# Kernel optimization log

Measured on AMD Instinct MI355X. Metric: run time of the kernel, lower is better.

## Reference

```python
import jax, jax.numpy as jnp
import numpy as np

EPS = 1e-5  # torch BatchNorm2d default eps
K = 3       # kernel_size
D = 1       # dilation (== padding)


def setup_inputs() -> dict:
    key = jax.random.key(0)
    k0, k1, k2 = jax.random.split(key, 3)
    N, C, H, W, O = 4, 2048, 32, 32, 256
    return {
        "x": jax.random.normal(k0, (N, C, H, W), jnp.float32),
        "conv_w": jax.random.normal(k1, (K * K, C, K, K), jnp.float32) * 0.01,
        "gamma": jnp.ones((K * K,), jnp.float32),
        "beta": jnp.zeros((K * K,), jnp.float32),
        "weight": jax.random.normal(k2, (O, C, K * K), jnp.float32) * 0.01,
    }


def reference(x, conv_w, gamma, beta, weight):
    n, c, h, w = x.shape
    # --- dynamic-kernel generator: conv (stride 1, pad=dilation) -> BN (train mode) -> softmax over K*K ---
    sigma = jax.lax.conv_general_dilated(
        x, conv_w, window_strides=(1, 1), padding=[(D, D), (D, D)],
        rhs_dilation=(D, D), dimension_numbers=("NCHW", "OIHW", "NCHW"))  # (n, K*K, h, w)
    mean = sigma.mean(axis=(0, 2, 3), keepdims=True)
    var = sigma.var(axis=(0, 2, 3), keepdims=True)  # biased variance, as torch BN uses for normalization
    sigma = (sigma - mean) * jax.lax.rsqrt(var + EPS)
    sigma = sigma * gamma[None, :, None, None] + beta[None, :, None, None]
    sigma = jax.nn.softmax(sigma, axis=1)            # softmax over the K*K kernel positions
    sigma = sigma.reshape(n, K * K, h * w)           # (n, K*K, h*w)
    # --- unfold (im2col), channel-major (C, kh, kw) ordering matching torch F.unfold ---
    patches = jax.lax.conv_general_dilated_patches(
        x, (K, K), (1, 1), [(D, D), (D, D)], rhs_dilation=(D, D),
        dimension_numbers=("NCHW", "OIHW", "NCHW"))  # (n, C*K*K, h, w)
    patches = patches.reshape(n, c, K * K, h * w)     # (n, C, K*K, h*w)
    # --- per-pixel dynamic weighting + learned projection ---
    # out[n,o,m] = sum_{c,l} patches[n,c,l,m] * sigma[n,l,m] * weight[o,c,l]
    out = jnp.einsum("nclm,nlm,ocl->nom", patches, sigma, weight)
    return out.reshape(n, weight.shape[0], h, w)
```

## Files before the change

### kernel.cpp

```cpp
#include <hip/hip_runtime.h>
#include <hip/hip_bf16.h>
#include <stdint.h>

typedef unsigned short u16;
typedef __attribute__((ext_vector_type(8))) short short8;
typedef __attribute__((ext_vector_type(4))) float floatx4;

#define N_IMG 4
#define C_IN  2048
#define HW    1024
#define KK    9
#define O_OUT 256
#define NPIX  4096
#define M_ROWS 2385
#define M_PAD  2432
#define K_DIM  2048
#define BN_EPS 1e-5f

#define OFF_A    0u
#define OFF_XT   9961472u
#define OFF_H    26738688u
#define OFF_SRAW 46661632u
#define OFF_SIG  46809088u
#define OFF_STAT 46956544u

__device__ __forceinline__ u16 f2b(float f) {
    unsigned u = __float_as_uint(f);
    return (u16)((u + 0x7FFFu + ((u >> 16) & 1u)) >> 16);
}

__device__ __forceinline__ void load8f(const float* base, size_t eidx, u16* out) {
    const float* p = base + eidx;
    float4 a = ((const float4*)p)[0];
    float4 b = ((const float4*)p)[1];
    float f[8] = {a.x, a.y, a.z, a.w, b.x, b.y, b.z, b.w};
#pragma unroll
    for (int j = 0; j < 8; ++j) out[j] = f2b(f[j]);
}

__global__ void build_xt(const float* __restrict__ x, u16* __restrict__ xt) {
    __shared__ __align__(16) u16 lds[64 * 72];
    int c0 = blockIdx.x * 64, p0 = blockIdx.y * 64, n = blockIdx.z;
    int t = threadIdx.x;
    int r = t >> 3, pv = (t & 7) * 8;
    u16 h0[8], h1[8];
    load8f(x, (size_t)(n * C_IN + c0 + r) * HW + p0 + pv, h0);
    load8f(x, (size_t)(n * C_IN + c0 + r + 32) * HW + p0 + pv, h1);
#pragma unroll
    for (int j = 0; j < 8; ++j) {
        lds[(pv + j) * 72 + r]      = h0[j];
        lds[(pv + j) * 72 + r + 32] = h1[j];
    }
    __syncthreads();
    int pr = t >> 3, cv = (t & 7) * 8;
    uint4 o0 = *(const uint4*)&lds[pr * 72 + cv];
    uint4 o1 = *(const uint4*)&lds[(pr + 32) * 72 + cv];
    *(uint4*)(xt + (size_t)(n * HW + p0 + pr) * K_DIM + c0 + cv) = o0;
    *(uint4*)(xt + (size_t)(n * HW + p0 + pr + 32) * K_DIM + c0 + cv) = o1;
}

__global__ void build_a(const float* __restrict__ wgt, const float* __restrict__ cw,
                        u16* __restrict__ A, float* __restrict__ stats) {
    __shared__ __align__(16) u16 lds[9 * 2056];
    int b = blockIdx.x, t = threadIdx.x;
    if (b < 256) {
        size_t base = (size_t)b * 18432;
        for (int i = 0; i < 9; ++i) {
            int e0 = (t + i * 256) * 8;
            u16 hv[8];
            load8f(wgt, base + e0, hv);
#pragma unroll
            for (int j = 0; j < 8; ++j) {
                int e = e0 + j;
                int c = e / 9, l = e - c * 9;
                lds[l * 2056 + c] = hv[j];
            }
        }
        __syncthreads();
        for (int l = 0; l < 9; ++l) {
            size_t row = (size_t)l * 256 + b;
            *(uint4*)(A + row * K_DIM + t * 8) = *(const uint4*)&lds[l * 2056 + t * 8];
        }
    } else if (b < 265) {
        int l = b - 256;
        size_t base = (size_t)l * 18432;
        for (int i = 0; i < 9; ++i) {
            int e0 = (t + i * 256) * 8;
            u16 hv[8];
            load8f(cw, base + e0, hv);
#pragma unroll
            for (int j = 0; j < 8; ++j) {
                int e = e0 + j;
                int c = e / 9, k = e - c * 9;
                lds[k * 2056 + c] = hv[j];
            }
        }
        __syncthreads();
        for (int k = 0; k < 9; ++k) {
            size_t row = 2304 + (size_t)k * 9 + l;
            *(uint4*)(A + row * K_DIM + t * 8) = *(const uint4*)&lds[k * 2056 + t * 8];
        }
    } else {
        uint4 z = {0, 0, 0, 0};
        uint4* dst = (uint4*)(A + (size_t)2385 * K_DIM);
        for (int i = t; i < (47 * 2048) / 8; i += 256) dst[i] = z;
        if (t < 18) stats[t] = 0.0f;
    }
}

__device__ __forceinline__ void gload_lds16(const void* g, void* l) {
    __builtin_amdgcn_global_load_lds((__attribute__((address_space(1))) void*)(g),
                                     (__attribute__((address_space(3))) void*)(l), 16, 0, 0);
}

__global__ void gemm_bt(const u16* __restrict__ A, const u16* __restrict__ B,
                        __hip_bfloat16* __restrict__ C) {
    __shared__ __align__(16) u16 As[128 * 32];
    __shared__ __align__(16) u16 Bs[128 * 32];
    int bx = blockIdx.x;
    int mt = bx % 19, nt = bx / 19;
    int m0 = mt * 128, n0 = nt * 128;
    int t = threadIdx.x;
    int w = t >> 6, lam = t & 63;
    int wm = w >> 1, wn = w & 1;
    int lm = lam & 15, q = lam >> 4;

    floatx4 acc[4][4];
    floatx4 z = {0.f, 0.f, 0.f, 0.f};
#pragma unroll
    for (int i = 0; i < 4; ++i)
#pragma unroll
        for (int j = 0; j < 4; ++j) acc[i][j] = z;

    int c0 = w, c1 = w + 4;
    int rrow0 = c0 * 16 + (lam >> 2);
    int rrow1 = c1 * 16 + (lam >> 2);
    int kc = (lam & 3) * 8;
    const u16* gA0 = A + (size_t)(m0 + rrow0) * K_DIM + kc;
    const u16* gA1 = A + (size_t)(m0 + rrow1) * K_DIM + kc;
    const u16* gB0 = B + (size_t)(n0 + rrow0) * K_DIM + kc;
    const u16* gB1 = B + (size_t)(n0 + rrow1) * K_DIM + kc;
    u16* lA0 = As + c0 * 512;  u16* lA1 = As + c1 * 512;
    u16* lB0 = Bs + c0 * 512;  u16* lB1 = Bs + c1 * 512;

    for (int kt = 0; kt < K_DIM / 32; ++kt) {
        gload_lds16(gA0, lA0);
        gload_lds16(gA1, lA1);
        gload_lds16(gB0, lB0);
        gload_lds16(gB1, lB1);
        gA0 += 32; gA1 += 32; gB0 += 32; gB1 += 32;
        __syncthreads();
        short8 af[4], bf[4];
#pragma unroll
        for (int i = 0; i < 4; ++i)
            af[i] = *(const short8*)(As + (wm * 64 + i * 16 + lm) * 32 + q * 8);
#pragma unroll
        for (int j = 0; j < 4; ++j)
            bf[j] = *(const short8*)(Bs + (wn * 64 + j * 16 + lm) * 32 + q * 8);
#pragma unroll
        for (int i = 0; i < 4; ++i)
#pragma unroll
            for (int j = 0; j < 4; ++j)
                acc[i][j] = __builtin_amdgcn_mfma_f32_16x16x32_bf16(af[i], bf[j], acc[i][j], 0, 0, 0);
        __syncthreads();
    }
#pragma unroll
    for (int i = 0; i < 4; ++i) {
        int gm = m0 + wm * 64 + i * 16 + q * 4;
#pragma unroll
        for (int j = 0; j < 4; ++j) {
            int gn = n0 + wn * 64 + j * 16 + lm;
#pragma unroll
            for (int r = 0; r < 4; ++r)
                C[(size_t)(gm + r) * NPIX + gn] = __float2bfloat16(acc[i][j][r]);
        }
    }
}

__global__ void sigma_stats(const __hip_bfloat16* __restrict__ Hm, float* __restrict__ sraw,
                            float* __restrict__ stats) {
    int b = blockIdx.x;
    int n = b / 9, l = b - n * 9;
    int t = threadIdx.x;
    float s1 = 0.f, s2 = 0.f;
    for (int i = 0; i < 4; ++i) {
        int pix = t + i * 256;
        int y = pix >> 5, x = pix & 31;
        float v = 0.f;
#pragma unroll
        for (int k = 0; k < 9; ++k) {
            int yy = y + k / 3 - 1, xx = x + (k % 3) - 1;
            if (yy >= 0 && yy < 32 && xx >= 0 && xx < 32)
                v += __bfloat162float(Hm[(size_t)(2304 + k * 9 + l) * NPIX + n * HW + yy * 32 + xx]);
        }
        sraw[(size_t)b * HW + pix] = v;
        s1 += v; s2 += v * v;
    }
    __shared__ float r1[256], r2[256];
    r1[t] = s1; r2[t] = s2;
    __syncthreads();
    for (int s = 128; s > 0; s >>= 1) {
        if (t < s) { r1[t] += r1[t + s]; r2[t] += r2[t + s]; }
        __syncthreads();
    }
    if (t == 0) { atomicAdd(&stats[l], r1[0]); atomicAdd(&stats[9 + l], r2[0]); }
}

__global__ void bn_softmax(const float* __restrict__ sraw, const float* __restrict__ stats,
                           const float* __restrict__ gamma, const float* __restrict__ beta,
                           float* __restrict__ sig) {
    int gid = blockIdx.x * 256 + threadIdx.x;
    int n = gid >> 10, pix = gid & 1023;
    float v[9];
    float mx = -1e30f;
#pragma unroll
    for (int l = 0; l < 9; ++l) {
        float mean = stats[l] * (1.f / 4096.f);
        float var  = stats[9 + l] * (1.f / 4096.f) - mean * mean;
        float tv = (sraw[(size_t)(n * 9 + l) * HW + pix] - mean) * rsqrtf(var + BN_EPS);
        tv = tv * gamma[l] + beta[l];
        v[l] = tv; mx = fmaxf(mx, tv);
    }
    float s = 0.f;
#pragma unroll
    for (int l = 0; l < 9; ++l) { v[l] = __expf(v[l] - mx); s += v[l]; }
    float inv = 1.f / s;
#pragma unroll
    for (int l = 0; l < 9; ++l) sig[(size_t)(n * 9 + l) * HW + pix] = v[l] * inv;
}

__global__ void epilogue(const __hip_bfloat16* __restrict__ Hm, const float* __restrict__ sig,
                         float* __restrict__ out) {
    int b = blockIdx.x;
    int n = b >> 8, o = b & 255;
    int t = threadIdx.x;
    for (int i = 0; i < 4; ++i) {
        int pix = t + i * 256;
        int y = pix >> 5, x = pix & 31;
        float acc = 0.f;
#pragma unroll
        for (int l = 0; l < 9; ++l) {
            int yy = y + l / 3 - 1, xx = x + (l % 3) - 1;
            if (yy >= 0 && yy < 32 && xx >= 0 && xx < 32) {
                float s = sig[(size_t)(n * 9 + l) * HW + pix];
                float h = __bfloat162float(Hm[(size_t)(l * 256 + o) * NPIX + n * HW + yy * 32 + xx]);
                acc += s * h;
            }
        }
        out[(size_t)b * HW + pix] = acc;
    }
}

extern "C" void kernel_launch(void* const* d_in, const int* in_sizes, int n_in,
                              void* d_out, int out_size, void* d_ws, size_t ws_size,
                              hipStream_t stream) {
    const float* x     = (const float*)d_in[0];
    const float* cw    = (const float*)d_in[1];
    const float* gamma = (const float*)d_in[2];
    const float* beta  = (const float*)d_in[3];
    const float* wgt   = (const float*)d_in[4];

    char* ws = (char*)d_ws;
    u16*   Abuf = (u16*)(ws + OFF_A);
    u16*   XT   = (u16*)(ws + OFF_XT);
    u16*   Hm   = (u16*)(ws + OFF_H);
    float* sraw = (float*)(ws + OFF_SRAW);
    float* sig  = (float*)(ws + OFF_SIG);
    float* stats= (float*)(ws + OFF_STAT);

    build_xt<<<dim3(C_IN / 64, HW / 64, N_IMG), 256, 0, stream>>>(x, XT);
    build_a<<<266, 256, 0, stream>>>(wgt, cw, Abuf, stats);
    gemm_bt<<<(M_PAD / 128) * (NPIX / 128), 256, 0, stream>>>(Abuf, XT, (__hip_bfloat16*)Hm);
    sigma_stats<<<N_IMG * KK, 256, 0, stream>>>((const __hip_bfloat16*)Hm, sraw, stats);
    bn_softmax<<<16, 256, 0, stream>>>(sraw, stats, gamma, beta, sig);
    epilogue<<<N_IMG * O_OUT, 256, 0, stream>>>((const __hip_bfloat16*)Hm, sig, (float*)d_out);
}
```

Measured before the change: 184.5 us.

## Merge prep kernels, halve GEMM N-tile, and split sigma stats across more blocks

Folds the x transpose/convert and the weight-packing kernels into one launch, which removes a launch and lets the two run together. The GEMM N tile drops from 128 to 64, doubling the grid to 1216 blocks so the MI355X's CUs are better filled, at the cost of more A reloads and lower per-block reuse. The sigma_stats kernel now uses four times as many blocks, one pixel per thread, in place of 36 blocks that each loop over pixels. That adds more atomics on the stats array.

```diff
diff --git a/kernel.cpp b/kernel.cpp
--- a/kernel.cpp
+++ b/kernel.cpp
@@ -38,33 +38,31 @@
     for (int j = 0; j < 8; ++j) out[j] = f2b(f[j]);
 }
 
-__global__ void build_xt(const float* __restrict__ x, u16* __restrict__ xt) {
-    __shared__ __align__(16) u16 lds[64 * 72];
-    int c0 = blockIdx.x * 64, p0 = blockIdx.y * 64, n = blockIdx.z;
-    int t = threadIdx.x;
-    int r = t >> 3, pv = (t & 7) * 8;
-    u16 h0[8], h1[8];
-    load8f(x, (size_t)(n * C_IN + c0 + r) * HW + p0 + pv, h0);
-    load8f(x, (size_t)(n * C_IN + c0 + r + 32) * HW + p0 + pv, h1);
-#pragma unroll
-    for (int j = 0; j < 8; ++j) {
-        lds[(pv + j) * 72 + r]      = h0[j];
-        lds[(pv + j) * 72 + r + 32] = h1[j];
-    }
-    __syncthreads();
-    int pr = t >> 3, cv = (t & 7) * 8;
-    uint4 o0 = *(const uint4*)&lds[pr * 72 + cv];
-    uint4 o1 = *(const uint4*)&lds[(pr + 32) * 72 + cv];
-    *(uint4*)(xt + (size_t)(n * HW + p0 + pr) * K_DIM + c0 + cv) = o0;
-    *(uint4*)(xt + (size_t)(n * HW + p0 + pr + 32) * K_DIM + c0 + cv) = o1;
-}
-
-__global__ void build_a(const float* __restrict__ wgt, const float* __restrict__ cw,
-                        u16* __restrict__ A, float* __restrict__ stats) {
+__global__ void build_all(const float* __restrict__ x, const float* __restrict__ wgt,
+                          const float* __restrict__ cw, u16* __restrict__ xt,
+                          u16* __restrict__ A, float* __restrict__ stats) {
     __shared__ __align__(16) u16 lds[9 * 2056];
     int b = blockIdx.x, t = threadIdx.x;
-    if (b < 256) {
-        size_t base = (size_t)b * 18432;
+    if (b < 2048) {
+        int c0 = (b & 31) * 64, p0 = ((b >> 5) & 15) * 64, n = b >> 9;
+        int r = t >> 3, pv = (t & 7) * 8;
+        u16 h0[8], h1[8];
+        load8f(x, (size_t)(n * C_IN + c0 + r) * HW + p0 + pv, h0);
+        load8f(x, (size_t)(n * C_IN + c0 + r + 32) * HW + p0 + pv, h1);
+#pragma unroll
+        for (int j = 0; j < 8; ++j) {
+            lds[(pv + j) * 72 + r]      = h0[j];
+            lds[(pv + j) * 72 + r + 32] = h1[j];
+        }
+        __syncthreads();
+        int pr = t >> 3, cv = (t & 7) * 8;
+        uint4 o0 = *(const uint4*)&lds[pr * 72 + cv];
+        uint4 o1 = *(const uint4*)&lds[(pr + 32) * 72 + cv];
+        *(uint4*)(xt + (size_t)(n * HW + p0 + pr) * K_DIM + c0 + cv) = o0;
+        *(uint4*)(xt + (size_t)(n * HW + p0 + pr + 32) * K_DIM + c0 + cv) = o1;
+    } else if (b < 2304) {
+        int o = b - 2048;
+        size_t base = (size_t)o * 18432;
         for (int i = 0; i < 9; ++i) {
             int e0 = (t + i * 256) * 8;
             u16 hv[8];
@@ -78,11 +76,11 @@
         }
         __syncthreads();
         for (int l = 0; l < 9; ++l) {
-            size_t row = (size_t)l * 256 + b;
+            size_t row = (size_t)l * 256 + o;
             *(uint4*)(A + row * K_DIM + t * 8) = *(const uint4*)&lds[l * 2056 + t * 8];
         }
-    } else if (b < 265) {
-        int l = b - 256;
+    } else if (b < 2313) {
+        int l = b - 2304;
         size_t base = (size_t)l * 18432;
         for (int i = 0; i < 9; ++i) {
             int e0 = (t + i * 256) * 8;
@@ -116,51 +114,47 @@
 __global__ void gemm_bt(const u16* __restrict__ A, const u16* __restrict__ B,
                         __hip_bfloat16* __restrict__ C) {
     __shared__ __align__(16) u16 As[128 * 32];
-    __shared__ __align__(16) u16 Bs[128 * 32];
+    __shared__ __align__(16) u16 Bs[64 * 32];
     int bx = blockIdx.x;
     int mt = bx % 19, nt = bx / 19;
-    int m0 = mt * 128, n0 = nt * 128;
+    int m0 = mt * 128, n0 = nt * 64;
     int t = threadIdx.x;
     int w = t >> 6, lam = t & 63;
     int wm = w >> 1, wn = w & 1;
     int lm = lam & 15, q = lam >> 4;
 
-    floatx4 acc[4][4];
+    floatx4 acc[4][2];
     floatx4 z = {0.f, 0.f, 0.f, 0.f};
 #pragma unroll
     for (int i = 0; i < 4; ++i)
 #pragma unroll
-        for (int j = 0; j < 4; ++j) acc[i][j] = z;
-
-    int c0 = w, c1 = w + 4;
-    int rrow0 = c0 * 16 + (lam >> 2);
-    int rrow1 = c1 * 16 + (lam >> 2);
+        for (int j = 0; j < 2; ++j) acc[i][j] = z;
+
+    int rsub = lam >> 2;
     int kc = (lam & 3) * 8;
-    const u16* gA0 = A + (size_t)(m0 + rrow0) * K_DIM + kc;
-    const u16* gA1 = A + (size_t)(m0 + rrow1) * K_DIM + kc;
-    const u16* gB0 = B + (size_t)(n0 + rrow0) * K_DIM + kc;
-    const u16* gB1 = B + (size_t)(n0 + rrow1) * K_DIM + kc;
-    u16* lA0 = As + c0 * 512;  u16* lA1 = As + c1 * 512;
-    u16* lB0 = Bs + c0 * 512;  u16* lB1 = Bs + c1 * 512;
+    const u16* gA0 = A + (size_t)(m0 + w * 16 + rsub) * K_DIM + kc;
+    const u16* gA1 = A + (size_t)(m0 + (w + 4) * 16 + rsub) * K_DIM + kc;
+    const u16* gB0 = B + (size_t)(n0 + w * 16 + rsub) * K_DIM + kc;
+    u16* lA0 = As + w * 512;  u16* lA1 = As + (w + 4) * 512;
+    u16* lB0 = Bs + w * 512;
 
     for (int kt = 0; kt < K_DIM / 32; ++kt) {
         gload_lds16(gA0, lA0);
         gload_lds16(gA1, lA1);
         gload_lds16(gB0, lB0);
-        gload_lds16(gB1, lB1);
-        gA0 += 32; gA1 += 32; gB0 += 32; gB1 += 32;
-        __syncthreads();
-        short8 af[4], bf[4];
+        gA0 += 32; gA1 += 32; gB0 += 32;
+        __syncthreads();
+        short8 af[4], bf[2];
 #pragma unroll
         for (int i = 0; i < 4; ++i)
             af[i] = *(const short8*)(As + (wm * 64 + i * 16 + lm) * 32 + q * 8);
 #pragma unroll
-        for (int j = 0; j < 4; ++j)
-            bf[j] = *(const short8*)(Bs + (wn * 64 + j * 16 + lm) * 32 + q * 8);
+        for (int j = 0; j < 2; ++j)
+            bf[j] = *(const short8*)(Bs + (wn * 32 + j * 16 + lm) * 32 + q * 8);
 #pragma unroll
         for (int i = 0; i < 4; ++i)
 #pragma unroll
-            for (int j = 0; j < 4; ++j)
+            for (int j = 0; j < 2; ++j)
                 acc[i][j] = __builtin_amdgcn_mfma_f32_16x16x32_bf16(af[i], bf[j], acc[i][j], 0, 0, 0);
         __syncthreads();
     }
@@ -168,8 +162,8 @@
     for (int i = 0; i < 4; ++i) {
         int gm = m0 + wm * 64 + i * 16 + q * 4;
 #pragma unroll
-        for (int j = 0; j < 4; ++j) {
-            int gn = n0 + wn * 64 + j * 16 + lm;
+        for (int j = 0; j < 2; ++j) {
+            int gn = n0 + wn * 32 + j * 16 + lm;
 #pragma unroll
             for (int r = 0; r < 4; ++r)
                 C[(size_t)(gm + r) * NPIX + gn] = __float2bfloat16(acc[i][j][r]);
@@ -180,24 +174,21 @@
 __global__ void sigma_stats(const __hip_bfloat16* __restrict__ Hm, float* __restrict__ sraw,
                             float* __restrict__ stats) {
     int b = blockIdx.x;
-    int n = b / 9, l = b - n * 9;
+    int qq = b & 3, nl = b >> 2;
+    int n = nl / 9, l = nl - n * 9;
     int t = threadIdx.x;
-    float s1 = 0.f, s2 = 0.f;
-    for (int i = 0; i < 4; ++i) {
-        int pix = t + i * 256;
-        int y = pix >> 5, x = pix & 31;
-        float v = 0.f;
-#pragma unroll
-        for (int k = 0; k < 9; ++k) {
-            int yy = y + k / 3 - 1, xx = x + (k % 3) - 1;
-            if (yy >= 0 && yy < 32 && xx >= 0 && xx < 32)
-                v += __bfloat162float(Hm[(size_t)(2304 + k * 9 + l) * NPIX + n * HW + yy * 32 + xx]);
-        }
-        sraw[(size_t)b * HW + pix] = v;
-        s1 += v; s2 += v * v;
-    }
+    int pix = qq * 256 + t;
+    int y = pix >> 5, x = pix & 31;
+    float v = 0.f;
+#pragma unroll
+    for (int k = 0; k < 9; ++k) {
+        int yy = y + k / 3 - 1, xx = x + (k % 3) - 1;
+        if (yy >= 0 && yy < 32 && xx >= 0 && xx < 32)
+            v += __bfloat162float(Hm[(size_t)(2304 + k * 9 + l) * NPIX + n * HW + yy * 32 + xx]);
+    }
+    sraw[(size_t)nl * HW + pix] = v;
     __shared__ float r1[256], r2[256];
-    r1[t] = s1; r2[t] = s2;
+    r1[t] = v; r2[t] = v * v;
     __syncthreads();
     for (int s = 128; s > 0; s >>= 1) {
         if (t < s) { r1[t] += r1[t + s]; r2[t] += r2[t + s]; }
@@ -268,10 +259,9 @@
     float* sig  = (float*)(ws + OFF_SIG);
     float* stats= (float*)(ws + OFF_STAT);
 
-    build_xt<<<dim3(C_IN / 64, HW / 64, N_IMG), 256, 0, stream>>>(x, XT);
-    build_a<<<266, 256, 0, stream>>>(wgt, cw, Abuf, stats);
-    gemm_bt<<<(M_PAD / 128) * (NPIX / 128), 256, 0, stream>>>(Abuf, XT, (__hip_bfloat16*)Hm);
-    sigma_stats<<<N_IMG * KK, 256, 0, stream>>>((const __hip_bfloat16*)Hm, sraw, stats);
+    build_all<<<2314, 256, 0, stream>>>(x, wgt, cw, XT, Abuf, stats);
+    gemm_bt<<<19 * 64, 256, 0, stream>>>(Abuf, XT, (__hip_bfloat16*)Hm);
+    sigma_stats<<<N_IMG * KK * 4, 256, 0, stream>>>((const __hip_bfloat16*)Hm, sraw, stats);
     bn_softmax<<<16, 256, 0, stream>>>(sraw, stats, gamma, beta, sig);
     epilogue<<<N_IMG * O_OUT, 256, 0, stream>>>((const __hip_bfloat16*)Hm, sig, (float*)d_out);
 }
```

Measured after the change: 199.4 us. 8.1% more time.

## Merge prep kernels and fuse sigma/BN/softmax/epilogue into one tail kernel

Applied to the files above, without the earlier changes.

Merges build_xt and build_a into one launch, and replaces the sigma_stats, bn_softmax and epilogue kernels with a single tail kernel. In the tail kernel every block recomputes the global BN statistics redundantly, which removes the atomics, the stats zeroing and the intermediate sraw/sig buffers. It then computes the softmax weights for its pixels and does the weighted projection for 64 output channels. The intent is to cut launch count and global round trips. The cost is that the tail runs only 64 blocks, each repeating the full statistics pass, which may underuse the GPU.

```diff
diff --git a/kernel.cpp b/kernel.cpp
--- a/kernel.cpp
+++ b/kernel.cpp
@@ -20,13 +20,13 @@
 #define OFF_A    0u
 #define OFF_XT   9961472u
 #define OFF_H    26738688u
-#define OFF_SRAW 46661632u
-#define OFF_SIG  46809088u
-#define OFF_STAT 46956544u
 
 __device__ __forceinline__ u16 f2b(float f) {
     unsigned u = __float_as_uint(f);
     return (u16)((u + 0x7FFFu + ((u >> 16) & 1u)) >> 16);
+}
+__device__ __forceinline__ float b2f(u16 h) {
+    return __uint_as_float(((unsigned)h) << 16);
 }
 
 __device__ __forceinline__ void load8f(const float* base, size_t eidx, u16* out) {
@@ -38,33 +38,31 @@
     for (int j = 0; j < 8; ++j) out[j] = f2b(f[j]);
 }
 
-__global__ void build_xt(const float* __restrict__ x, u16* __restrict__ xt) {
-    __shared__ __align__(16) u16 lds[64 * 72];
-    int c0 = blockIdx.x * 64, p0 = blockIdx.y * 64, n = blockIdx.z;
-    int t = threadIdx.x;
-    int r = t >> 3, pv = (t & 7) * 8;
-    u16 h0[8], h1[8];
-    load8f(x, (size_t)(n * C_IN + c0 + r) * HW + p0 + pv, h0);
-    load8f(x, (size_t)(n * C_IN + c0 + r + 32) * HW + p0 + pv, h1);
-#pragma unroll
-    for (int j = 0; j < 8; ++j) {
-        lds[(pv + j) * 72 + r]      = h0[j];
-        lds[(pv + j) * 72 + r + 32] = h1[j];
-    }
-    __syncthreads();
-    int pr = t >> 3, cv = (t & 7) * 8;
-    uint4 o0 = *(const uint4*)&lds[pr * 72 + cv];
-    uint4 o1 = *(const uint4*)&lds[(pr + 32) * 72 + cv];
-    *(uint4*)(xt + (size_t)(n * HW + p0 + pr) * K_DIM + c0 + cv) = o0;
-    *(uint4*)(xt + (size_t)(n * HW + p0 + pr + 32) * K_DIM + c0 + cv) = o1;
-}
-
-__global__ void build_a(const float* __restrict__ wgt, const float* __restrict__ cw,
-                        u16* __restrict__ A, float* __restrict__ stats) {
+__global__ void build_all(const float* __restrict__ x, const float* __restrict__ wgt,
+                          const float* __restrict__ cw, u16* __restrict__ xt,
+                          u16* __restrict__ A) {
     __shared__ __align__(16) u16 lds[9 * 2056];
     int b = blockIdx.x, t = threadIdx.x;
-    if (b < 256) {
-        size_t base = (size_t)b * 18432;
+    if (b < 2048) {
+        int c0 = (b & 31) * 64, p0 = ((b >> 5) & 15) * 64, n = b >> 9;
+        int r = t >> 3, pv = (t & 7) * 8;
+        u16 h0[8], h1[8];
+        load8f(x, (size_t)(n * C_IN + c0 + r) * HW + p0 + pv, h0);
+        load8f(x, (size_t)(n * C_IN + c0 + r + 32) * HW + p0 + pv, h1);
+#pragma unroll
+        for (int j = 0; j < 8; ++j) {
+            lds[(pv + j) * 72 + r]      = h0[j];
+            lds[(pv + j) * 72 + r + 32] = h1[j];
+        }
+        __syncthreads();
+        int pr = t >> 3, cv = (t & 7) * 8;
+        uint4 o0 = *(const uint4*)&lds[pr * 72 + cv];
+        uint4 o1 = *(const uint4*)&lds[(pr + 32) * 72 + cv];
+        *(uint4*)(xt + (size_t)(n * HW + p0 + pr) * K_DIM + c0 + cv) = o0;
+        *(uint4*)(xt + (size_t)(n * HW + p0 + pr + 32) * K_DIM + c0 + cv) = o1;
+    } else if (b < 2304) {
+        int o = b - 2048;
+        size_t base = (size_t)o * 18432;
         for (int i = 0; i < 9; ++i) {
             int e0 = (t + i * 256) * 8;
             u16 hv[8];
@@ -78,11 +76,11 @@
         }
         __syncthreads();
         for (int l = 0; l < 9; ++l) {
-            size_t row = (size_t)l * 256 + b;
+            size_t row = (size_t)l * 256 + o;
             *(uint4*)(A + row * K_DIM + t * 8) = *(const uint4*)&lds[l * 2056 + t * 8];
         }
-    } else if (b < 265) {
-        int l = b - 256;
+    } else if (b < 2313) {
+        int l = b - 2304;
         size_t base = (size_t)l * 18432;
         for (int i = 0; i < 9; ++i) {
             int e0 = (t + i * 256) * 8;
@@ -104,7 +102,6 @@
         uint4 z = {0, 0, 0, 0};
         uint4* dst = (uint4*)(A + (size_t)2385 * K_DIM);
         for (int i = t; i < (47 * 2048) / 8; i += 256) dst[i] = z;
-        if (t < 18) stats[t] = 0.0f;
     }
 }
 
@@ -148,7 +145,7 @@
         gload_lds16(gA1, lA1);
         gload_lds16(gB0, lB0);
         gload_lds16(gB1, lB1);
-        gA0 += 32; gA1 += 32; gB0 += 32; gB1 += 32;
+        gA0 += 32; gA1 += 32; gB0 += 32;  gB1 += 32;
         __syncthreads();
         short8 af[4], bf[4];
 #pragma unroll
@@ -177,77 +174,105 @@
     }
 }
 
-__global__ void sigma_stats(const __hip_bfloat16* __restrict__ Hm, float* __restrict__ sraw,
-                            float* __restrict__ stats) {
+__global__ void tail_fused(const __hip_bfloat16* __restrict__ Hm, const float* __restrict__ gamma,
+                           const float* __restrict__ beta, float* __restrict__ out) {
+    __shared__ float redbuf[4][18];
+    __shared__ float statS[18];
     int b = blockIdx.x;
-    int n = b / 9, l = b - n * 9;
+    int nb = b >> 4, pc = (b >> 2) & 3, oc = b & 3;
     int t = threadIdx.x;
-    float s1 = 0.f, s2 = 0.f;
-    for (int i = 0; i < 4; ++i) {
-        int pix = t + i * 256;
-        int y = pix >> 5, x = pix & 31;
-        float v = 0.f;
-#pragma unroll
-        for (int k = 0; k < 9; ++k) {
-            int yy = y + k / 3 - 1, xx = x + (k % 3) - 1;
-            if (yy >= 0 && yy < 32 && xx >= 0 && xx < 32)
-                v += __bfloat162float(Hm[(size_t)(2304 + k * 9 + l) * NPIX + n * HW + yy * 32 + xx]);
-        }
-        sraw[(size_t)b * HW + pix] = v;
-        s1 += v; s2 += v * v;
-    }
-    __shared__ float r1[256], r2[256];
-    r1[t] = s1; r2[t] = s2;
+
+    float s1[9], s2[9];
+#pragma unroll
+    for (int l = 0; l < 9; ++l) { s1[l] = 0.f; s2[l] = 0.f; }
+    for (int n = 0; n < 4; ++n) {
+        for (int i = 0; i < 4; ++i) {
+            int pix = i * 256 + t;
+            int y = pix >> 5, x = pix & 31;
+            float v[9];
+#pragma unroll
+            for (int l = 0; l < 9; ++l) v[l] = 0.f;
+#pragma unroll
+            for (int k = 0; k < 9; ++k) {
+                int dy = k / 3 - 1, dx = k % 3 - 1;
+                int yy = y + dy, xx = x + dx;
+                bool ok = (yy >= 0 && yy < 32 && xx >= 0 && xx < 32);
+                int sp = ok ? (pix + dy * 32 + dx) : pix;
+                float m = ok ? 1.f : 0.f;
+                const __hip_bfloat16* base = Hm + (size_t)(2304 + k * 9) * NPIX + n * HW + sp;
+#pragma unroll
+                for (int l = 0; l < 9; ++l)
+                    v[l] += m * __bfloat162float(base[(size_t)l * NPIX]);
+            }
+#pragma unroll
+            for (int l = 0; l < 9; ++l) { s1[l] += v[l]; s2[l] += v[l] * v[l]; }
+        }
+    }
+#pragma unroll
+    for (int l = 0; l < 9; ++l) {
+        for (int off = 32; off > 0; off >>= 1) {
+            s1[l] += __shfl_down(s1[l], off, 64);
+            s2[l] += __shfl_down(s2[l], off, 64);
+        }
+    }
+    int wv = t >> 6, lane = t & 63;
+    if (lane == 0) {
+#pragma unroll
+        for (int l = 0; l < 9; ++l) { redbuf[wv][l] = s1[l]; redbuf[wv][9 + l] = s2[l]; }
+    }
     __syncthreads();
-    for (int s = 128; s > 0; s >>= 1) {
-        if (t < s) { r1[t] += r1[t + s]; r2[t] += r2[t + s]; }
-        __syncthreads();
-    }
-    if (t == 0) { atomicAdd(&stats[l], r1[0]); atomicAdd(&stats[9 + l], r2[0]); }
-}
-
-__global__ void bn_softmax(const float* __restrict__ sraw, const float* __restrict__ stats,
-                           const float* __restrict__ gamma, const float* __restrict__ beta,
-                           float* __restrict__ sig) {
-    int gid = blockIdx.x * 256 + threadIdx.x;
-    int n = gid >> 10, pix = gid & 1023;
+    if (t < 18) statS[t] = redbuf[0][t] + redbuf[1][t] + redbuf[2][t] + redbuf[3][t];
+    __syncthreads();
+
+    int pix = pc * 256 + t;
+    int y = pix >> 5, x = pix & 31;
     float v[9];
+#pragma unroll
+    for (int l = 0; l < 9; ++l) v[l] = 0.f;
+#pragma unroll
+    for (int k = 0; k < 9; ++k) {
+        int dy = k / 3 - 1, dx = k % 3 - 1;
+        int yy = y + dy, xx = x + dx;
+        bool ok = (yy >= 0 && yy < 32 && xx >= 0 && xx < 32);
+        int sp = ok ? (pix + dy * 32 + dx) : pix;
+        float m = ok ? 1.f : 0.f;
+        const __hip_bfloat16* base = Hm + (size_t)(2304 + k * 9) * NPIX + nb * HW + sp;
+#pragma unroll
+        for (int l = 0; l < 9; ++l)
+            v[l] += m * __bfloat162float(base[(size_t)l * NPIX]);
+    }
     float mx = -1e30f;
 #pragma unroll
     for (int l = 0; l < 9; ++l) {
-        float mean = stats[l] * (1.f / 4096.f);
-        float var  = stats[9 + l] * (1.f / 4096.f) - mean * mean;
-        float tv = (sraw[(size_t)(n * 9 + l) * HW + pix] - mean) * rsqrtf(var + BN_EPS);
+        float mean = statS[l] * (1.f / 4096.f);
+        float var  = statS[9 + l] * (1.f / 4096.f) - mean * mean;
+        float tv = (v[l] - mean) * rsqrtf(var + BN_EPS);
         tv = tv * gamma[l] + beta[l];
         v[l] = tv; mx = fmaxf(mx, tv);
     }
-    float s = 0.f;
-#pragma unroll
-    for (int l = 0; l < 9; ++l) { v[l] = __expf(v[l] - mx); s += v[l]; }
-    float inv = 1.f / s;
-#pragma unroll
-    for (int l = 0; l < 9; ++l) sig[(size_t)(n * 9 + l) * HW + pix] = v[l] * inv;
-}
-
-__global__ void epilogue(const __hip_bfloat16* __restrict__ Hm, const float* __restrict__ sig,
-                         float* __restrict__ out) {
-    int b = blockIdx.x;
-    int n = b >> 8, o = b & 255;
-    int t = threadIdx.x;
-    for (int i = 0; i < 4; ++i) {
-        int pix = t + i * 256;
-        int y = pix >> 5, x = pix & 31;
+    float ssum = 0.f;
+#pragma unroll
+    for (int l = 0; l < 9; ++l) { v[l] = __expf(v[l] - mx); ssum += v[l]; }
+    float inv = 1.f / ssum;
+
+    float sv[9]; int sp[9];
+#pragma unroll
+    for (int l = 0; l < 9; ++l) {
+        int dy = l / 3 - 1, dx = l % 3 - 1;
+        int yy = y + dy, xx = x + dx;
+        bool ok = (yy >= 0 && yy < 32 && xx >= 0 && xx < 32);
+        sp[l] = ok ? (pix + dy * 32 + dx) : pix;
+        sv[l] = ok ? v[l] * inv : 0.f;
+    }
+    const __hip_bfloat16* hb = Hm + (size_t)nb * HW;
+    float* ob = out + ((size_t)nb * 256 + oc * 64) * HW + pix;
+    for (int o = 0; o < 64; ++o) {
+        int oo = oc * 64 + o;
         float acc = 0.f;
 #pragma unroll
-        for (int l = 0; l < 9; ++l) {
-            int yy = y + l / 3 - 1, xx = x + (l % 3) - 1;
-            if (yy >= 0 && yy < 32 && xx >= 0 && xx < 32) {
-                float s = sig[(size_t)(n * 9 + l) * HW + pix];
-                float h = __bfloat162float(Hm[(size_t)(l * 256 + o) * NPIX + n * HW + yy * 32 + xx]);
-                acc += s * h;
-            }
-        }
-        out[(size_t)b * HW + pix] = acc;
+        for (int l = 0; l < 9; ++l)
+            acc += sv[l] * __bfloat162float(hb[(size_t)(l * 256 + oo) * NPIX + sp[l]]);
+        ob[(size_t)o * HW] = acc;
     }
 }
 
@@ -261,17 +286,11 @@
     const float* wgt   = (const float*)d_in[4];
 
     char* ws = (char*)d_ws;
-    u16*   Abuf = (u16*)(ws + OFF_A);
-    u16*   XT   = (u16*)(ws + OFF_XT);
-    u16*   Hm   = (u16*)(ws + OFF_H);
-    float* sraw = (float*)(ws + OFF_SRAW);
-    float* sig  = (float*)(ws + OFF_SIG);
-    float* stats= (float*)(ws + OFF_STAT);
-
-    build_xt<<<dim3(C_IN / 64, HW / 64, N_IMG), 256, 0, stream>>>(x, XT);
-    build_a<<<266, 256, 0, stream>>>(wgt, cw, Abuf, stats);
-    gemm_bt<<<(M_PAD / 128) * (NPIX / 128), 256, 0, stream>>>(Abuf, XT, (__hip_bfloat16*)Hm);
-    sigma_stats<<<N_IMG * KK, 256, 0, stream>>>((const __hip_bfloat16*)Hm, sraw, stats);
-    bn_softmax<<<16, 256, 0, stream>>>(sraw, stats, gamma, beta, sig);
-    epilogue<<<N_IMG * O_OUT, 256, 0, stream>>>((const __hip_bfloat16*)Hm, sig, (float*)d_out);
-}
+    u16* Abuf = (u16*)(ws + OFF_A);
+    u16* XT   = (u16*)(ws + OFF_XT);
+    u16* Hm   = (u16*)(ws + OFF_H);
+
+    build_all<<<2314, 256, 0, stream>>>(x, wgt, cw, XT, Abuf);
+    gemm_bt<<<19 * 32, 256, 0, stream>>>(Abuf, XT, (__hip_bfloat16*)Hm);
+    tail_fused<<<64, 256, 0, stream>>>((const __hip_bfloat16*)Hm, gamma, beta, (float*)d_out);
+}
```

Measured after the change: 200.2 us. 1.09x slower.
